# Performance work log

Measured on AMD Instinct MI355X. Metric: run time of the kernel, lower is better.

The kernel has to match this reference:

```python
import jax, jax.numpy as jnp
import numpy as np

B = 16384          # number of bags / MLP batch
L = 50             # indices per bag (uniform offsets)
N = B * L          # total indices
V = 10_000_000     # num_embeddings
D = 3              # embedding dim (fixed by EmbeddingBag(num_embeddings, 3))
K = 13             # MLP input width


def setup_inputs() -> dict:
    key = jax.random.key(0)
    ks = jax.random.split(key, 10)
    eb_input = jax.random.randint(ks[0], (N,), 0, V, dtype=jnp.int32)
    eb_offset = (jnp.arange(B, dtype=jnp.int32) * L)  # sorted, starts at 0
    mlp_input = jax.random.normal(ks[1], (B, K), dtype=jnp.float32)
    # single shared table: [EmbeddingBag]*3 in torch aliases one module
    emb_weight = jax.random.normal(ks[2], (V, D), dtype=jnp.float32) * 0.01
    w0 = jax.random.normal(ks[3], (12, K), dtype=jnp.float32) * (1.0 / np.sqrt(K))
    b0 = jax.random.normal(ks[4], (12,), dtype=jnp.float32) * 0.01
    w1 = jax.random.normal(ks[5], (6, 12), dtype=jnp.float32) * (1.0 / np.sqrt(12))
    b1 = jax.random.normal(ks[6], (6,), dtype=jnp.float32) * 0.01
    w2 = jax.random.normal(ks[7], (3, 6), dtype=jnp.float32) * (1.0 / np.sqrt(6))
    b2 = jax.random.normal(ks[8], (3,), dtype=jnp.float32) * 0.01
    return {"eb_input": eb_input, "eb_offset": eb_offset, "mlp_input": mlp_input,
            "emb_weight": emb_weight, "w0": w0, "b0": b0,
            "w1": w1, "b1": b1, "w2": w2, "b2": b2}


def _embedding_bag_mean(weight, indices, offsets, num_bags):
    # torch EmbeddingBag default mode='mean': per-bag mean of gathered rows
    n = indices.shape[0]
    # bag id for every index position (generic variable-offset handling)
    bag_ids = jnp.searchsorted(offsets, jnp.arange(n, dtype=offsets.dtype), side='right') - 1
    gathered = weight[indices]                                   # [N, D]
    sums = jax.ops.segment_sum(gathered, bag_ids, num_segments=num_bags)  # [B, D]
    counts = jnp.diff(jnp.append(offsets, n)).astype(weight.dtype)        # [B]
    return sums / counts[:, None]


def reference(eb_input, eb_offset, mlp_input, emb_weight, w0, b0, w1, b1, w2, b2):
    eb_out = _embedding_bag_mean(emb_weight, eb_input, eb_offset, B)  # [B, 3]
    # three EmbeddingBag calls share the same weight => identical outputs
    h = mlp_input @ w0.T + b0
    h = h @ w1.T + b1
    mlp_out = h @ w2.T + b2                                           # [B, 3]
    return jnp.concatenate([eb_out, eb_out, eb_out, mlp_out], axis=1)  # [B, 12]
```

## Files before the change

### kernel.cpp

```cpp
#include <hip/hip_runtime.h>

#define BAGS   16384
#define DIM    3
#define KIN    13

__global__ __launch_bounds__(256) void eb_kernel(
    const int* __restrict__ idxs, const int* __restrict__ offs,
    const float* __restrict__ W, float* __restrict__ out, int n_total)
{
    int wave = (int)((blockIdx.x * blockDim.x + threadIdx.x) >> 6);
    int lane = (int)(threadIdx.x & 63);
    if (wave >= BAGS) return;

    int start = offs[wave];
    int end   = (wave + 1 < BAGS) ? offs[wave + 1] : n_total;
    int cnt   = end - start;

    float s0 = 0.f, s1 = 0.f, s2 = 0.f;
    for (int i = start + lane; i < end; i += 64) {
        int idx = idxs[i];
        const float* row = W + (size_t)idx * DIM;
        s0 += row[0];
        s1 += row[1];
        s2 += row[2];
    }

    #pragma unroll
    for (int off = 32; off > 0; off >>= 1) {
        s0 += __shfl_down(s0, off);
        s1 += __shfl_down(s1, off);
        s2 += __shfl_down(s2, off);
    }

    if (lane == 0) {
        float inv = 1.0f / (float)cnt;
        float e0 = s0 * inv, e1 = s1 * inv, e2 = s2 * inv;
        float* o = out + (size_t)wave * 12;
        o[0] = e0; o[1] = e1; o[2] = e2;
        o[3] = e0; o[4] = e1; o[5] = e2;
        o[6] = e0; o[7] = e1; o[8] = e2;
    }
}

__global__ __launch_bounds__(256) void mlp_kernel(
    const float* __restrict__ x,
    const float* __restrict__ w0, const float* __restrict__ b0,
    const float* __restrict__ w1, const float* __restrict__ b1,
    const float* __restrict__ w2, const float* __restrict__ b2,
    float* __restrict__ out)
{
    int b = (int)(blockIdx.x * blockDim.x + threadIdx.x);
    if (b >= BAGS) return;

    float xi[KIN];
    #pragma unroll
    for (int k = 0; k < KIN; ++k) xi[k] = x[(size_t)b * KIN + k];

    float h0[12];
    #pragma unroll
    for (int j = 0; j < 12; ++j) {
        float acc = b0[j];
        #pragma unroll
        for (int k = 0; k < KIN; ++k) acc += w0[j * KIN + k] * xi[k];
        h0[j] = acc;
    }

    float h1[6];
    #pragma unroll
    for (int j = 0; j < 6; ++j) {
        float acc = b1[j];
        #pragma unroll
        for (int k = 0; k < 12; ++k) acc += w1[j * 12 + k] * h0[k];
        h1[j] = acc;
    }

    float* o = out + (size_t)b * 12 + 9;
    #pragma unroll
    for (int j = 0; j < 3; ++j) {
        float acc = b2[j];
        #pragma unroll
        for (int k = 0; k < 6; ++k) acc += w2[j * 6 + k] * h1[k];
        o[j] = acc;
    }
}

extern "C" void kernel_launch(void* const* d_in, const int* in_sizes, int n_in,
                              void* d_out, int out_size, void* d_ws, size_t ws_size,
                              hipStream_t stream) {
    const int*   eb_input   = (const int*)  d_in[0];
    const int*   eb_offset  = (const int*)  d_in[1];
    const float* mlp_input  = (const float*)d_in[2];
    const float* emb_weight = (const float*)d_in[3];
    const float* w0 = (const float*)d_in[4];
    const float* b0 = (const float*)d_in[5];
    const float* w1 = (const float*)d_in[6];
    const float* b1 = (const float*)d_in[7];
    const float* w2 = (const float*)d_in[8];
    const float* b2 = (const float*)d_in[9];
    float* out = (float*)d_out;

    int n_total = in_sizes[0];

    int eb_blocks = BAGS / 4;
    eb_kernel<<<eb_blocks, 256, 0, stream>>>(eb_input, eb_offset, emb_weight, out, n_total);

    int mlp_blocks = (BAGS + 255) / 256;
    mlp_kernel<<<mlp_blocks, 256, 0, stream>>>(mlp_input, w0, b0, w1, b1, w2, b2, out);
}
```

Before: 27.69 us.

## Fuse embedding-bag and MLP kernels, use 16-lane groups per bag

```diff
diff --git a/kernel.cpp b/kernel.cpp
--- a/kernel.cpp
+++ b/kernel.cpp
@@ -1,86 +1,103 @@
 #include <hip/hip_runtime.h>
 
-#define BAGS   16384
-#define DIM    3
-#define KIN    13
+#define BAGS       16384
+#define KIN        13
+#define EB_BLOCKS  1024
+#define MLP_BLOCKS 64
 
-__global__ __launch_bounds__(256) void eb_kernel(
+__global__ __launch_bounds__(256) void fused_kernel(
     const int* __restrict__ idxs, const int* __restrict__ offs,
-    const float* __restrict__ W, float* __restrict__ out, int n_total)
-{
-    int wave = (int)((blockIdx.x * blockDim.x + threadIdx.x) >> 6);
-    int lane = (int)(threadIdx.x & 63);
-    if (wave >= BAGS) return;
-
-    int start = offs[wave];
-    int end   = (wave + 1 < BAGS) ? offs[wave + 1] : n_total;
-    int cnt   = end - start;
-
-    float s0 = 0.f, s1 = 0.f, s2 = 0.f;
-    for (int i = start + lane; i < end; i += 64) {
-        int idx = idxs[i];
-        const float* row = W + (size_t)idx * DIM;
-        s0 += row[0];
-        s1 += row[1];
-        s2 += row[2];
-    }
-
-    #pragma unroll
-    for (int off = 32; off > 0; off >>= 1) {
-        s0 += __shfl_down(s0, off);
-        s1 += __shfl_down(s1, off);
-        s2 += __shfl_down(s2, off);
-    }
-
-    if (lane == 0) {
-        float inv = 1.0f / (float)cnt;
-        float e0 = s0 * inv, e1 = s1 * inv, e2 = s2 * inv;
-        float* o = out + (size_t)wave * 12;
-        o[0] = e0; o[1] = e1; o[2] = e2;
-        o[3] = e0; o[4] = e1; o[5] = e2;
-        o[6] = e0; o[7] = e1; o[8] = e2;
-    }
-}
-
-__global__ __launch_bounds__(256) void mlp_kernel(
-    const float* __restrict__ x,
+    const float* __restrict__ W, const float* __restrict__ x,
     const float* __restrict__ w0, const float* __restrict__ b0,
     const float* __restrict__ w1, const float* __restrict__ b1,
     const float* __restrict__ w2, const float* __restrict__ b2,
-    float* __restrict__ out)
+    float* __restrict__ out, int n_total)
 {
-    int b = (int)(blockIdx.x * blockDim.x + threadIdx.x);
-    if (b >= BAGS) return;
+    if (blockIdx.x < EB_BLOCKS) {
+        int tid = (int)(blockIdx.x * 256 + threadIdx.x);
+        int bag = tid >> 4;
+        int sl  = (int)(threadIdx.x & 15);
 
-    float xi[KIN];
-    #pragma unroll
-    for (int k = 0; k < KIN; ++k) xi[k] = x[(size_t)b * KIN + k];
+        int start = offs[bag];
+        int end   = (bag + 1 < BAGS) ? offs[bag + 1] : n_total;
+        int cnt   = end - start;
 
-    float h0[12];
-    #pragma unroll
-    for (int j = 0; j < 12; ++j) {
-        float acc = b0[j];
+        float s0 = 0.f, s1 = 0.f, s2 = 0.f;
+
+        if (cnt == 50) {
+            int i0 = start + sl;
+            int ia = idxs[i0];
+            int ib = idxs[i0 + 16];
+            int ic = idxs[i0 + 32];
+            const float* ra = W + (size_t)ia * 3;
+            const float* rb = W + (size_t)ib * 3;
+            const float* rc = W + (size_t)ic * 3;
+            float a0 = ra[0], a1 = ra[1], a2 = ra[2];
+            float e0 = rb[0], e1 = rb[1], e2 = rb[2];
+            float c0 = rc[0], c1 = rc[1], c2 = rc[2];
+            s0 = a0 + e0 + c0;
+            s1 = a1 + e1 + c1;
+            s2 = a2 + e2 + c2;
+            if (sl < 2) {
+                int idd = idxs[i0 + 48];
+                const float* rd = W + (size_t)idd * 3;
+                s0 += rd[0]; s1 += rd[1]; s2 += rd[2];
+            }
+        } else {
+            for (int i = start + sl; i < end; i += 16) {
+                int idx = idxs[i];
+                const float* r = W + (size_t)idx * 3;
+                s0 += r[0]; s1 += r[1]; s2 += r[2];
+            }
+        }
+
         #pragma unroll
-        for (int k = 0; k < KIN; ++k) acc += w0[j * KIN + k] * xi[k];
-        h0[j] = acc;
-    }
+        for (int m = 8; m >= 1; m >>= 1) {
+            s0 += __shfl_xor(s0, m, 16);
+            s1 += __shfl_xor(s1, m, 16);
+            s2 += __shfl_xor(s2, m, 16);
+        }
 
-    float h1[6];
-    #pragma unroll
-    for (int j = 0; j < 6; ++j) {
-        float acc = b1[j];
+        if (sl < 9) {
+            float inv = 1.0f / (float)cnt;
+            int c = sl % 3;
+            float e = (c == 0 ? s0 : (c == 1 ? s1 : s2)) * inv;
+            out[(size_t)bag * 12 + sl] = e;
+        }
+    } else {
+        int b = (int)((blockIdx.x - EB_BLOCKS) * 256 + threadIdx.x);
+        if (b >= BAGS) return;
+
+        float xi[KIN];
         #pragma unroll
-        for (int k = 0; k < 12; ++k) acc += w1[j * 12 + k] * h0[k];
-        h1[j] = acc;
-    }
+        for (int k = 0; k < KIN; ++k) xi[k] = x[(size_t)b * KIN + k];
 
-    float* o = out + (size_t)b * 12 + 9;
-    #pragma unroll
-    for (int j = 0; j < 3; ++j) {
-        float acc = b2[j];
+        float h0[12];
         #pragma unroll
-        for (int k = 0; k < 6; ++k) acc += w2[j * 6 + k] * h1[k];
-        o[j] = acc;
+        for (int j = 0; j < 12; ++j) {
+            float acc = b0[j];
+            #pragma unroll
+            for (int k = 0; k < KIN; ++k) acc += w0[j * KIN + k] * xi[k];
+            h0[j] = acc;
+        }
+
+        float h1[6];
+        #pragma unroll
+        for (int j = 0; j < 6; ++j) {
+            float acc = b1[j];
+            #pragma unroll
+            for (int k = 0; k < 12; ++k) acc += w1[j * 12 + k] * h0[k];
+            h1[j] = acc;
+        }
+
+        float* o = out + (size_t)b * 12 + 9;
+        #pragma unroll
+        for (int j = 0; j < 3; ++j) {
+            float acc = b2[j];
+            #pragma unroll
+            for (int k = 0; k < 6; ++k) acc += w2[j * 6 + k] * h1[k];
+            o[j] = acc;
+        }
     }
 }
 
@@ -101,9 +118,7 @@
 
     int n_total = in_sizes[0];
 
-    int eb_blocks = BAGS / 4;
-    eb_kernel<<<eb_blocks, 256, 0, stream>>>(eb_input, eb_offset, emb_weight, out, n_total);
-
-    int mlp_blocks = (BAGS + 255) / 256;
-    mlp_kernel<<<mlp_blocks, 256, 0, stream>>>(mlp_input, w0, b0, w1, b1, w2, b2, out);
+    fused_kernel<<<EB_BLOCKS + MLP_BLOCKS, 256, 0, stream>>>(
+        eb_input, eb_offset, emb_weight, mlp_input,
+        w0, b0, w1, b1, w2, b2, out, n_total);
 }
```

Result: faster. 24.63 us (-11.1%).
